# Kernel optimization log

Measured on AMD Instinct MI355X. Metric: run time of the kernel, lower is better.

The kernel has to match this reference:

```python
import jax, jax.numpy as jnp
import numpy as np

B, N, NDIM = 256, 127, 3          # batch, particles, input features
D, H, L, HID = 256, 8, 4, 256     # d_model, heads, layers, dim_feedforward(=nb_features=head hidden)
M = HID                           # Performer nb_features
DH = D // H                       # head dim
LN_EPS = 1e-5
KERN_EPS = 1e-4


def leaky(x):
    return jnp.where(x >= 0, x, 0.2 * x)


def layer_norm(x, g, b):
    mu = jnp.mean(x, axis=-1, keepdims=True)
    var = jnp.mean((x - mu) ** 2, axis=-1, keepdims=True)
    return (x - mu) * jax.lax.rsqrt(var + LN_EPS) * g + b


def softmax_kernel(data, proj, is_query):
    # FAVOR+ positive softmax random features (performer_pytorch.softmax_kernel)
    # data [B,H,S,DH], proj [M,DH]
    normalizer = DH ** -0.25
    ratio = proj.shape[0] ** -0.5
    dd = jnp.einsum('bhnd,md->bhnm', data * normalizer, proj)
    diag = jnp.sum(data ** 2, axis=-1, keepdims=True) * 0.5 * (normalizer ** 2)
    if is_query:
        mx = jax.lax.stop_gradient(jnp.max(dd, axis=-1, keepdims=True))
    else:
        mx = jax.lax.stop_gradient(jnp.max(dd))
    return ratio * (jnp.exp(dd - diag - mx) + KERN_EPS)


def performer_attn(h, keep, Wq, bq, Wk, bk, Wv, bv, Wo, bo, proj):
    Bc, S, _ = h.shape
    def split(y):
        return y.reshape(Bc, S, H, DH).transpose(0, 2, 1, 3)  # [B,H,S,DH]
    q = split(jnp.einsum('bnd,ed->bne', h, Wq) + bq)
    k = split(jnp.einsum('bnd,ed->bne', h, Wk) + bk)
    v = split(jnp.einsum('bnd,ed->bne', h, Wv) + bv) * keep   # zero padded values
    qp = softmax_kernel(q, proj, True)    # [B,H,S,M]
    kp = softmax_kernel(k, proj, False)   # [B,H,S,M]
    ksum = jnp.sum(kp, axis=2)                                   # [B,H,M]
    d_inv = 1.0 / jnp.einsum('bhnm,bhm->bhn', qp, ksum)          # [B,H,S]
    ctx = jnp.einsum('bhnm,bhnd->bhmd', kp, v)                   # [B,H,M,DH]
    o = jnp.einsum('bhmd,bhnm,bhn->bhnd', ctx, qp, d_inv)
    o = o.transpose(0, 2, 1, 3).reshape(Bc, S, D)
    return jnp.einsum('bnd,ed->bne', o, Wo) + bo


def encoder_layer(h, keep, Wq, bq, Wk, bk, Wv, bv, Wo, bo, proj,
                  n1w, n1b, n2w, n2b, f1w, f1b, f2w, f2b):
    # NOTE: the repo's override drops the residual connections (post-norm, no skip)
    a = performer_attn(h, keep, Wq, bq, Wk, bk, Wv, bv, Wo, bo, proj)
    h = layer_norm(a, n1w, n1b)
    f = jnp.einsum('bnh,dh->bnd', leaky(jnp.einsum('bnd,hd->bnh', h, f1w) + f1b), f2w) + f2b
    return layer_norm(f, n2w, n2b)


def setup_inputs():
    key = jax.random.key(0)
    ks = jax.random.split(key, 32)
    s = 0.02
    def w(k, shape):
        return jax.random.normal(k, shape, jnp.float32) * s
    return {
        'x': jax.random.normal(ks[0], (B, N, NDIM), jnp.float32),
        'mask': jax.random.randint(ks[1], (B, N), 0, 2) == 1,
        'emb_w': w(ks[2], (D, NDIM)), 'emb_b': w(ks[3], (D,)),
        'Wq': w(ks[4], (L, D, D)), 'bq': w(ks[5], (L, D)),
        'Wk': w(ks[6], (L, D, D)), 'bk': w(ks[7], (L, D)),
        'Wv': w(ks[8], (L, D, D)), 'bv': w(ks[9], (L, D)),
        'Wo': w(ks[10], (L, D, D)), 'bo': w(ks[11], (L, D)),
        'proj': jax.random.normal(ks[12], (L, M, DH), jnp.float32),
        'n1w': jnp.ones((L, D)), 'n1b': jnp.zeros((L, D)),
        'n2w': jnp.ones((L, D)), 'n2b': jnp.zeros((L, D)),
        'f1w': w(ks[13], (L, HID, D)), 'f1b': w(ks[14], (L, HID)),
        'f2w': w(ks[15], (L, D, HID)), 'f2b': w(ks[16], (L, D)),
        'h1w': w(ks[17], (2 * HID, D)), 'h1b': w(ks[18], (2 * HID,)),
        'h2w': w(ks[19], (HID, 2 * HID)), 'h2b': w(ks[20], (HID,)),
        'ow': w(ks[21], (1, HID)), 'ob': w(ks[22], (1,)),
    }


def reference(x, mask, emb_w, emb_b, Wq, bq, Wk, bk, Wv, bv, Wo, bo, proj,
              n1w, n1b, n2w, n2b, f1w, f1b, f2w, f2b,
              h1w, h1b, h2w, h2b, ow, ob):
    h = jnp.einsum('bnf,df->bnd', x, emb_w) + emb_b               # embed [B,N,D]
    h = jnp.concatenate([jnp.zeros_like(h[:, :1]), h], axis=1)    # prepend zero CLS token
    pad = jnp.concatenate([jnp.zeros_like(mask[:, :1]), mask], axis=1)  # [B,N+1], True=pad
    keep = (~pad).astype(h.dtype)[:, None, :, None]               # [B,1,S,1]
    for l in range(L):
        h = encoder_layer(h, keep, Wq[l], bq[l], Wk[l], bk[l], Wv[l], bv[l],
                          Wo[l], bo[l], proj[l], n1w[l], n1b[l], n2w[l], n2b[l],
                          f1w[l], f1b[l], f2w[l], f2b[l])
    c = h[:, 0]                                                   # CLS token [B,D]
    c = leaky(jnp.einsum('bd,hd->bh', c, h1w) + h1b)
    c = leaky(jnp.einsum('bh,gh->bg', c, h2w) + h2b)
    return jnp.einsum('bg,og->bo', c, ow) + ob                    # [B,1]
```

## Files before the change

kernel.cpp:

```cpp
#include <hip/hip_runtime.h>
#include <math.h>

#define B_ 256
#define N_ 127
#define S_ 128
#define NDIM_ 3
#define D_ 256
#define H_ 8
#define DH_ 32
#define M_ 256
#define HID_ 256
#define L_ 4
#define LOG2E 1.44269504088896340736f

typedef __attribute__((ext_vector_type(8))) short short8;
typedef __attribute__((ext_vector_type(4))) short bfx4;
typedef __attribute__((ext_vector_type(4))) float floatx4;

__device__ __forceinline__ ushort bf16_rn(float x) {
    unsigned u = __float_as_uint(x);
    u = (u + 0x7fffu + ((u >> 16) & 1u)) >> 16;
    return (ushort)u;
}
__device__ __forceinline__ unsigned split_pack(float x) {
    const ushort h = bf16_rn(x);
    const float r = x - __uint_as_float(((unsigned)h) << 16);
    const ushort l = bf16_rn(r);
    return (unsigned)h | ((unsigned)l << 16);
}
__device__ __forceinline__ float rec(unsigned u) {
    return __uint_as_float(u << 16) + __uint_as_float(u & 0xffff0000u);
}
__device__ __forceinline__ unsigned hpair(unsigned u0, unsigned u1) {
    return (u0 & 0xffffu) | (u1 << 16);
}
__device__ __forceinline__ unsigned lpair(unsigned u0, unsigned u1) {
    return (u0 >> 16) | (u1 & 0xffff0000u);
}

__device__ __forceinline__ float blk_sum(float v, float* sred) {
#pragma unroll
    for (int o = 32; o > 0; o >>= 1) v += __shfl_xor(v, o, 64);
    if ((threadIdx.x & 63) == 0) sred[threadIdx.x >> 6] = v;
    __syncthreads();
    v = sred[0] + sred[1] + sred[2] + sred[3];
    __syncthreads();
    return v;
}

__global__ void __launch_bounds__(256) k_prep(
    const float* __restrict__ Wq, const float* __restrict__ Wk, const float* __restrict__ Wv,
    const float* __restrict__ Wo, const float* __restrict__ f1w, const float* __restrict__ f2w,
    const float* __restrict__ proj, ushort* __restrict__ WH, ushort* __restrict__ WL,
    unsigned* __restrict__ P2, int* __restrict__ slots,
    const float* __restrict__ x, const float* __restrict__ ew, const float* __restrict__ eb,
    unsigned* __restrict__ Aout)
{
    const int bid = blockIdx.x;
    if (bid < 768) {
        const int tensor = bid / 128;
        const int tid = (bid & 127) * 256 + threadIdx.x;
        const float* src = tensor == 0 ? Wq : tensor == 1 ? Wk : tensor == 2 ? Wv
                         : tensor == 3 ? Wo : tensor == 4 ? f1w : f2w;
        ushort* dh = WH + (size_t)tensor * L_ * 65536;
        ushort* dl = WL + (size_t)tensor * L_ * 65536;
        const int l = tid >> 13;
        const int col = (tid >> 5) & 255, kc = tid & 31;
        const float* sp = src + ((size_t)l << 16) + col * 256 + kc * 8;
        float v[8];
        *(float4*)&v[0] = *(const float4*)sp;
        *(float4*)&v[4] = *(const float4*)(sp + 4);
        unsigned hu[4], lu[4];
#pragma unroll
        for (int i = 0; i < 4; i++) {
            const unsigned u0 = split_pack(v[2 * i]);
            const unsigned u1 = split_pack(v[2 * i + 1]);
            hu[i] = hpair(u0, u1);
            lu[i] = lpair(u0, u1);
        }
        const size_t off = ((size_t)l << 16) + ((size_t)(kc * 256 + col)) * 8;
        *(uint4*)&dh[off] = make_uint4(hu[0], hu[1], hu[2], hu[3]);
        *(uint4*)&dl[off] = make_uint4(lu[0], lu[1], lu[2], lu[3]);
    } else if (bid < 800) {
        const int idx = ((bid - 768) * 256 + threadIdx.x) * 4;
        const float4 w4 = *(const float4*)&proj[idx];
        const float v[4] = {w4.x, w4.y, w4.z, w4.w};
        unsigned u[4];
#pragma unroll
        for (int i = 0; i < 4; i++) u[i] = split_pack(v[i]);
        *(uint4*)&P2[idx] = make_uint4(u[0], u[1], u[2], u[3]);
    } else if (bid == 800) {
        if (threadIdx.x < 4) {
            const int i = __float_as_int(-INFINITY);
            slots[threadIdx.x] = (i >= 0) ? i : (i ^ 0x7fffffff);
        }
    } else {
        const int idx4 = (bid - 801) * 256 + threadIdx.x;
        const int d0 = (idx4 & 63) * 4;
        const int n = (idx4 >> 6) & (S_ - 1);
        const int b = idx4 >> 13;
        unsigned r[4] = {0u, 0u, 0u, 0u};
        if (n > 0) {
            const float* xr = x + ((size_t)b * N_ + (n - 1)) * NDIM_;
            const float x0 = xr[0], x1 = xr[1], x2 = xr[2];
#pragma unroll
            for (int j = 0; j < 4; j++) {
                const int d = d0 + j;
                const float val = eb[d] + x0 * ew[d * 3 + 0] + x1 * ew[d * 3 + 1] + x2 * ew[d * 3 + 2];
                r[j] = split_pack(val);
            }
        }
        *(uint4*)&Aout[(size_t)idx4 * 4] = make_uint4(r[0], r[1], r[2], r[3]);
    }
}

__global__ void __launch_bounds__(512, 2) k_gemm_qkv(
    const unsigned* __restrict__ Ap, const ushort* __restrict__ WHb,
    const ushort* __restrict__ WLb, const int l,
    const float* __restrict__ bq, const float* __restrict__ bk, const float* __restrict__ bv_,
    const int* __restrict__ mask,
    unsigned* __restrict__ Qo, unsigned* __restrict__ Ko, unsigned* __restrict__ Vo)
{
    __shared__ ushort sAh[2][4160];
    __shared__ ushort sAl[2][4160];
    const int t = threadIdx.x;
    const int w = t >> 6, lane = t & 63;
    const int quad = lane >> 4, l16 = lane & 15;
    const int rowbase = 64 * (w >> 2), colbase = 64 * (w & 3);
    const int which = blockIdx.x >> 8;
    const int row0 = (blockIdx.x & 255) * 128;
    const ushort* WH = WHb + ((size_t)(which * L_ + l)) * 65536;
    const ushort* WL = WLb + ((size_t)(which * L_ + l)) * 65536;
    const float* bias = which == 0 ? bq : which == 1 ? bk : bv_;
    unsigned* out = which == 0 ? Qo : which == 1 ? Ko : Vo;

    floatx4 acc[4][4];
#pragma unroll
    for (int rt = 0; rt < 4; rt++)
#pragma unroll
        for (int ct = 0; ct < 4; ct++) acc[rt][ct] = (floatx4){0.f, 0.f, 0.f, 0.f};

    const int arow = t >> 2, achunk = t & 3;
    const unsigned* AG = Ap + (size_t)(row0 + arow) * D_ + achunk * 8;
    const int aidx = achunk * 1040 + arow * 8;

    {
        const uint4 a0 = *(const uint4*)AG;
        const uint4 a1 = *(const uint4*)(AG + 4);
        *(uint4*)&sAh[0][aidx] = make_uint4(hpair(a0.x, a0.y), hpair(a0.z, a0.w),
                                            hpair(a1.x, a1.y), hpair(a1.z, a1.w));
        *(uint4*)&sAl[0][aidx] = make_uint4(lpair(a0.x, a0.y), lpair(a0.z, a0.w),
                                            lpair(a1.x, a1.y), lpair(a1.z, a1.w));
    }
    __syncthreads();

    for (int s = 0; s < 8; s++) {
        const int p = s & 1;
        uint4 a0n, a1n;
        if (s + 1 < 8) {
            a0n = *(const uint4*)(AG + (s + 1) * 32);
            a1n = *(const uint4*)(AG + (s + 1) * 32 + 4);
        }
        const size_t wbase = ((size_t)((s * 4 + quad) * 256 + colbase + l16)) * 8;
        const ushort* WHf = WH + wbase;
        const ushort* WLf = WL + wbase;
        short8 ah[4], al[4], wh[4], wl[4];
#pragma unroll
        for (int ct = 0; ct < 4; ct++) {
            wh[ct] = *(const short8*)&WHf[ct * 128];
            wl[ct] = *(const short8*)&WLf[ct * 128];
        }
#pragma unroll
        for (int rt = 0; rt < 4; rt++) {
            const int ai = quad * 1040 + (rowbase + 16 * rt + l16) * 8;
            ah[rt] = *(const short8*)&sAh[p][ai];
            al[rt] = *(const short8*)&sAl[p][ai];
        }
#pragma unroll
        for (int rt = 0; rt < 4; rt++)
#pragma unroll
            for (int ct = 0; ct < 4; ct++) {
                acc[rt][ct] = __builtin_amdgcn_mfma_f32_16x16x32_bf16(ah[rt], wh[ct], acc[rt][ct], 0, 0, 0);
                acc[rt][ct] = __builtin_amdgcn_mfma_f32_16x16x32_bf16(ah[rt], wl[ct], acc[rt][ct], 0, 0, 0);
                acc[rt][ct] = __builtin_amdgcn_mfma_f32_16x16x32_bf16(al[rt], wh[ct], acc[rt][ct], 0, 0, 0);
            }
        if (s + 1 < 8) {
            *(uint4*)&sAh[p ^ 1][aidx] = make_uint4(hpair(a0n.x, a0n.y), hpair(a0n.z, a0n.w),
                                                    hpair(a1n.x, a1n.y), hpair(a1n.z, a1n.w));
            *(uint4*)&sAl[p ^ 1][aidx] = make_uint4(lpair(a0n.x, a0n.y), lpair(a0n.z, a0n.w),
                                                    lpair(a1n.x, a1n.y), lpair(a1n.z, a1n.w));
        }
        __syncthreads();
    }

    int colv[4]; float bv[4];
#pragma unroll
    for (int ct = 0; ct < 4; ct++) { colv[ct] = colbase + 16 * ct + l16; bv[ct] = bias[colv[ct]]; }

    const int b = row0 >> 7;
#pragma unroll
    for (int rt = 0; rt < 4; rt++)
#pragma unroll
    for (int i = 0; i < 4; i++) {
        const int rl = rowbase + 16 * rt + quad * 4 + i;
        const int n = (row0 + rl) & (S_ - 1);
        float keep = 1.f;
        if (which == 2) keep = (n == 0) ? 1.f : (mask[b * N_ + n - 1] ? 0.f : 1.f);
#pragma unroll
        for (int ct = 0; ct < 4; ct++) {
            float c = acc[rt][ct][i] + bv[ct];
            c *= keep;
            const int col = colv[ct];
            out[(((size_t)b * H_ + (col >> 5)) * S_ + n) * DH_ + (col & 31)] = split_pack(c);
        }
    }
}

__global__ void __launch_bounds__(512, 2) k_wofn(
    const unsigned* __restrict__ Ap,
    const ushort* __restrict__ WoH, const ushort* __restrict__ WoL,
    const ushort* __restrict__ W1H, const ushort* __restrict__ W1L,
    const ushort* __restrict__ W2H, const ushort* __restrict__ W2L,
    const float* __restrict__ bo, const float* __restrict__ n1w, const float* __restrict__ n1b,
    const float* __restrict__ b1, const float* __restrict__ b2,
    const float* __restrict__ g2w, const float* __restrict__ g2b,
    unsigned* __restrict__ out)
{
    __shared__ char smemc[67584];
    ushort* Th  = (ushort*)smemc;
    ushort* Tl  = (ushort*)(smemc + 33792);
    ushort* sTh = (ushort*)smemc;
    ushort* sTl = (ushort*)(smemc + 8320);
    __shared__ float sredA[64][8], sredB[64][8];
    const int t = threadIdx.x;
    const int w = t >> 6, lane = t & 63;
    const int quad = lane >> 4, l16 = lane & 15;
    const int row0 = blockIdx.x * 64;

    floatx4 acc[2][4];
#pragma unroll
    for (int rt = 0; rt < 2; rt++)
#pragma unroll
        for (int ct = 0; ct < 4; ct++) acc[rt][ct] = (floatx4){0.f, 0.f, 0.f, 0.f};

    const int arow = t >> 3, akq = t & 7;
    const unsigned* AG = Ap + (size_t)(row0 + arow) * D_ + akq * 4;
    const int aidx = (akq >> 1) * 520 + arow * 8 + (akq & 1) * 4;

    {
        const uint4 a4 = *(const uint4*)AG;
        *(uint2*)&sTh[aidx] = make_uint2(hpair(a4.x, a4.y), hpair(a4.z, a4.w));
        *(uint2*)&sTl[aidx] = make_uint2(lpair(a4.x, a4.y), lpair(a4.z, a4.w));
    }
    __syncthreads();

    for (int s = 0; s < 8; s++) {
        const int p = s & 1;
        uint4 a_n;
        if (s + 1 < 8) a_n = *(const uint4*)(AG + (s + 1) * 32);
        const size_t wbase = ((size_t)((s * 4 + quad) * 256 + 32 * w + l16)) * 8;
        short8 fh[2], fl[2], th[4], tl[4];
#pragma unroll
        for (int rt = 0; rt < 2; rt++) {
            fh[rt] = *(const short8*)&WoH[wbase + rt * 128];
            fl[rt] = *(const short8*)&WoL[wbase + rt * 128];
        }
#pragma unroll
        for (int ct = 0; ct < 4; ct++) {
            const int ti = p * 2080 + quad * 520 + (16 * ct + l16) * 8;
            th[ct] = *(const short8*)&sTh[ti];
            tl[ct] = *(const short8*)&sTl[ti];
        }
#pragma unroll
        for (int rt = 0; rt < 2; rt++)
#pragma unroll
            for (int ct = 0; ct < 4; ct++) {
                acc[rt][ct] = __builtin_amdgcn_mfma_f32_16x16x32_bf16(fh[rt], th[ct], acc[rt][ct], 0, 0, 0);
                acc[rt][ct] = __builtin_amdgcn_mfma_f32_16x16x32_bf16(fl[rt], th[ct], acc[rt][ct], 0, 0, 0);
                acc[rt][ct] = __builtin_amdgcn_mfma_f32_16x16x32_bf16(fh[rt], tl[ct], acc[rt][ct], 0, 0, 0);
            }
        if (s + 1 < 8) {
            *(uint2*)&sTh[(p ^ 1) * 2080 + aidx] = make_uint2(hpair(a_n.x, a_n.y), hpair(a_n.z, a_n.w));
            *(uint2*)&sTl[(p ^ 1) * 2080 + aidx] = make_uint2(lpair(a_n.x, a_n.y), lpair(a_n.z, a_n.w));
        }
        __syncthreads();
    }

    {
        float bov[2][4];
#pragma unroll
        for (int rt = 0; rt < 2; rt++)
#pragma unroll
            for (int i = 0; i < 4; i++) bov[rt][i] = bo[32 * w + 16 * rt + quad * 4 + i];
        float ps[4], ps2[4];
#pragma unroll
        for (int ct = 0; ct < 4; ct++) { ps[ct] = 0.f; ps2[ct] = 0.f; }
#pragma unroll
        for (int rt = 0; rt < 2; rt++)
#pragma unroll
        for (int ct = 0; ct < 4; ct++)
#pragma unroll
        for (int i = 0; i < 4; i++) {
            const float c = acc[rt][ct][i] + bov[rt][i];
            acc[rt][ct][i] = c;
            ps[ct] += c; ps2[ct] += c * c;
        }
#pragma unroll
        for (int ct = 0; ct < 4; ct++) {
            ps[ct] += __shfl_xor(ps[ct], 16, 64);  ps[ct] += __shfl_xor(ps[ct], 32, 64);
            ps2[ct] += __shfl_xor(ps2[ct], 16, 64); ps2[ct] += __shfl_xor(ps2[ct], 32, 64);
        }
        if (quad == 0) {
#pragma unroll
            for (int ct = 0; ct < 4; ct++) {
                sredA[16 * ct + l16][w] = ps[ct];
                sredB[16 * ct + l16][w] = ps2[ct];
            }
        }
        __syncthreads();
        float mu[4], rs[4];
#pragma unroll
        for (int ct = 0; ct < 4; ct++) {
            const int n = 16 * ct + l16;
            float s = 0.f, s2 = 0.f;
#pragma unroll
            for (int k = 0; k < 8; k++) { s += sredA[n][k]; s2 += sredB[n][k]; }
            mu[ct] = s * (1.f / D_);
            rs[ct] = rsqrtf(s2 * (1.f / D_) - mu[ct] * mu[ct] + 1e-5f);
        }
        float gv1[2][4], bv1[2][4];
#pragma unroll
        for (int rt = 0; rt < 2; rt++)
#pragma unroll
            for (int i = 0; i < 4; i++) {
                const int c2 = 32 * w + 16 * rt + quad * 4 + i;
                gv1[rt][i] = n1w[c2];
                bv1[rt][i] = n1b[c2];
            }
#pragma unroll
        for (int ct = 0; ct < 4; ct++) {
            const int n = 16 * ct + l16;
#pragma unroll
            for (int rt = 0; rt < 2; rt++) {
                unsigned u[4];
#pragma unroll
                for (int i = 0; i < 4; i++) {
                    const float tv = (acc[rt][ct][i] - mu[ct]) * rs[ct] * gv1[rt][i] + bv1[rt][i];
                    u[i] = split_pack(tv);
                }
                const int base = n * 264 + 32 * w + 16 * rt + quad * 4;
                *(uint2*)&Th[base] = make_uint2(hpair(u[0], u[1]), hpair(u[2], u[3]));
                *(uint2*)&Tl[base] = make_uint2(lpair(u[0], u[1]), lpair(u[2], u[3]));
            }
        }
        __syncthreads();
    }

    floatx4 acc1[2][4];
#pragma unroll
    for (int rt = 0; rt < 2; rt++)
#pragma unroll
        for (int ct = 0; ct < 4; ct++) acc1[rt][ct] = (floatx4){0.f, 0.f, 0.f, 0.f};

    for (int s = 0; s < 8; s++) {
        const size_t wbase = ((size_t)((s * 4 + quad) * 256 + 32 * w + l16)) * 8;
        short8 fh[2], fl[2], th[4], tl[4];
#pragma unroll
        for (int rt = 0; rt < 2; rt++) {
            fh[rt] = *(const short8*)&W1H[wbase + rt * 128];
            fl[rt] = *(const short8*)&W1L[wbase + rt * 128];
        }
#pragma unroll
        for (int ct = 0; ct < 4; ct++) {
            const int ti = (16 * ct + l16) * 264 + s * 32 + quad * 8;
            th[ct] = *(const short8*)&Th[ti];
            tl[ct] = *(const short8*)&Tl[ti];
        }
#pragma unroll
        for (int rt = 0; rt < 2; rt++)
#pragma unroll
            for (int ct = 0; ct < 4; ct++) {
                acc1[rt][ct] = __builtin_amdgcn_mfma_f32_16x16x32_bf16(fh[rt], th[ct], acc1[rt][ct], 0, 0, 0);
                acc1[rt][ct] = __builtin_amdgcn_mfma_f32_16x16x32_bf16(fl[rt], th[ct], acc1[rt][ct], 0, 0, 0);
                acc1[rt][ct] = __builtin_amdgcn_mfma_f32_16x16x32_bf16(fh[rt], tl[ct], acc1[rt][ct], 0, 0, 0);
            }
    }
    __syncthreads();

    {
        float b1v[2][4];
#pragma unroll
        for (int rt = 0; rt < 2; rt++)
#pragma unroll
            for (int i = 0; i < 4; i++) b1v[rt][i] = b1[32 * w + 16 * rt + quad * 4 + i];
#pragma unroll
        for (int ct = 0; ct < 4; ct++) {
            const int n = 16 * ct + l16;
#pragma unroll
            for (int rt = 0; rt < 2; rt++) {
                unsigned u[4];
#pragma unroll
                for (int i = 0; i < 4; i++) {
                    float c = acc1[rt][ct][i] + b1v[rt][i];
                    c = (c >= 0.f) ? c : 0.2f * c;
                    u[i] = split_pack(c);
                }
                const int base = n * 264 + 32 * w + 16 * rt + quad * 4;
                *(uint2*)&Th[base] = make_uint2(hpair(u[0], u[1]), hpair(u[2], u[3]));
                *(uint2*)&Tl[base] = make_uint2(lpair(u[0], u[1]), lpair(u[2], u[3]));
            }
        }
        __syncthreads();
    }

    const int rowbase = 32 * (w >> 2), colbase = 64 * (w & 3);
    const int colg = w & 3;
    floatx4 acc2[2][4];
#pragma unroll
    for (int rt = 0; rt < 2; rt++)
#pragma unroll
        for (int ct = 0; ct < 4; ct++) acc2[rt][ct] = (floatx4){0.f, 0.f, 0.f, 0.f};

    for (int ks = 0; ks < 8; ks++) {
        const size_t w2base = ((size_t)((ks * 4 + quad) * 256 + colbase + l16)) * 8;
        short8 ah[2], al[2], wh[4], wl[4];
#pragma unroll
        for (int ct = 0; ct < 4; ct++) {
            wh[ct] = *(const short8*)&W2H[w2base + ct * 128];
            wl[ct] = *(const short8*)&W2L[w2base + ct * 128];
        }
#pragma unroll
        for (int rt = 0; rt < 2; rt++) {
            const int gi = (rowbase + 16 * rt + l16) * 264 + ks * 32 + quad * 8;
            ah[rt] = *(const short8*)&Th[gi];
            al[rt] = *(const short8*)&Tl[gi];
        }
#pragma unroll
        for (int rt = 0; rt < 2; rt++)
#pragma unroll
            for (int ct = 0; ct < 4; ct++) {
                acc2[rt][ct] = __builtin_amdgcn_mfma_f32_16x16x32_bf16(ah[rt], wh[ct], acc2[rt][ct], 0, 0, 0);
                acc2[rt][ct] = __builtin_amdgcn_mfma_f32_16x16x32_bf16(ah[rt], wl[ct], acc2[rt][ct], 0, 0, 0);
                acc2[rt][ct] = __builtin_amdgcn_mfma_f32_16x16x32_bf16(al[rt], wh[ct], acc2[rt][ct], 0, 0, 0);
            }
    }
    __syncthreads();

    int colv[4]; float bv[4], gv[4], bbv[4];
#pragma unroll
    for (int ct = 0; ct < 4; ct++) {
        colv[ct] = colbase + 16 * ct + l16;
        bv[ct] = b2[colv[ct]];
        gv[ct] = g2w[colv[ct]];
        bbv[ct] = g2b[colv[ct]];
    }
#pragma unroll
    for (int rt = 0; rt < 2; rt++)
#pragma unroll
    for (int i = 0; i < 4; i++) {
        const int rl = rowbase + 16 * rt + quad * 4 + i;
        float s = 0.f, s2 = 0.f;
#pragma unroll
        for (int ct = 0; ct < 4; ct++) {
            const float c = acc2[rt][ct][i] + bv[ct];
            s += c; s2 += c * c;
        }
#pragma unroll
        for (int o = 8; o > 0; o >>= 1) { s += __shfl_xor(s, o, 64); s2 += __shfl_xor(s2, o, 64); }
        if (l16 == 0) { sredA[rl][colg] = s; sredB[rl][colg] = s2; }
    }
    __syncthreads();
#pragma unroll
    for (int rt = 0; rt < 2; rt++)
#pragma unroll
    for (int i = 0; i < 4; i++) {
        const int rl = rowbase + 16 * rt + quad * 4 + i;
        const float s = sredA[rl][0] + sredA[rl][1] + sredA[rl][2] + sredA[rl][3];
        const float s2 = sredB[rl][0] + sredB[rl][1] + sredB[rl][2] + sredB[rl][3];
        const float mu = s * (1.f / D_);
        const float rs = rsqrtf(s2 * (1.f / D_) - mu * mu + 1e-5f);
#pragma unroll
        for (int ct = 0; ct < 4; ct++) {
            const float c = acc2[rt][ct][i] + bv[ct];
            out[(size_t)(row0 + rl) * D_ + colv[ct]] = split_pack((c - mu) * rs * gv[ct] + bbv[ct]);
        }
    }
}

__global__ void __launch_bounds__(256) k_dmax(
    const unsigned* __restrict__ kg, const unsigned* __restrict__ P2, int* __restrict__ slot)
{
    __shared__ __align__(16) ushort A2s[64 * 40];
    __shared__ __align__(16) ushort Ps[256 * 40];
    __shared__ float sred[4];
    const int t = threadIdx.x;
    const size_t row0 = (size_t)blockIdx.x * 64;
    {
        const int row = t >> 2, seg = t & 3;
        const unsigned* src = kg + (row0 + row) * DH_ + seg * 8;
        const uint4 f0 = *(const uint4*)src;
        const uint4 f1 = *(const uint4*)(src + 4);
        *(uint4*)&A2s[row * 40 + seg * 8] =
            make_uint4(hpair(f0.x, f0.y), hpair(f0.z, f0.w), hpair(f1.x, f1.y), hpair(f1.z, f1.w));
    }
    {
        const int col = t;
        const unsigned* src = P2 + (size_t)col * DH_;
#pragma unroll
        for (int hf = 0; hf < 2; hf++) {
            const uint4 g0 = *(const uint4*)(src + hf * 16);
            const uint4 g1 = *(const uint4*)(src + hf * 16 + 4);
            const uint4 g2 = *(const uint4*)(src + hf * 16 + 8);
            const uint4 g3 = *(const uint4*)(src + hf * 16 + 12);
            *(uint4*)&Ps[col * 40 + hf * 16] =
                make_uint4(hpair(g0.x, g0.y), hpair(g0.z, g0.w), hpair(g1.x, g1.y), hpair(g1.z, g1.w));
            *(uint4*)&Ps[col * 40 + hf * 16 + 8] =
                make_uint4(hpair(g2.x, g2.y), hpair(g2.z, g2.w), hpair(g3.x, g3.y), hpair(g3.z, g3.w));
        }
    }
    __syncthreads();
    const int w = t >> 6, lane = t & 63, quad = lane >> 4, l16 = lane & 15;
    floatx4 acc[4][4];
#pragma unroll
    for (int rt = 0; rt < 4; rt++)
#pragma unroll
        for (int ct = 0; ct < 4; ct++) acc[rt][ct] = (floatx4){0.f, 0.f, 0.f, 0.f};
    short8 af[4], bf[4];
#pragma unroll
    for (int rt = 0; rt < 4; rt++)
        af[rt] = *(const short8*)&A2s[(rt * 16 + l16) * 40 + quad * 8];
#pragma unroll
    for (int ct = 0; ct < 4; ct++)
        bf[ct] = *(const short8*)&Ps[((w * 4 + ct) * 16 + l16) * 40 + quad * 8];
#pragma unroll
    for (int rt = 0; rt < 4; rt++)
#pragma unroll
        for (int ct = 0; ct < 4; ct++)
            acc[rt][ct] = __builtin_amdgcn_mfma_f32_16x16x32_bf16(af[rt], bf[ct], acc[rt][ct], 0, 0, 0);
    float mx = -INFINITY;
#pragma unroll
    for (int rt = 0; rt < 4; rt++)
#pragma unroll
        for (int ct = 0; ct < 4; ct++)
#pragma unroll
            for (int i = 0; i < 4; i++) mx = fmaxf(mx, acc[rt][ct][i]);
#pragma unroll
    for (int o = 32; o > 0; o >>= 1) mx = fmaxf(mx, __shfl_xor(mx, o, 64));
    if (lane == 0) sred[w] = mx;
    __syncthreads();
    if (t == 0) {
        const float m4 = fmaxf(fmaxf(sred[0], sred[1]), fmaxf(sred[2], sred[3]))
                       * 0.42044820762685725f;
        const int i = __float_as_int(m4);
        atomicMax(slot, (i >= 0) ? i : (i ^ 0x7fffffff));
    }
}

__global__ void __launch_bounds__(1024) k_attn2(
    const unsigned* __restrict__ qg, const unsigned* __restrict__ kg, const unsigned* __restrict__ vg,
    const unsigned* __restrict__ P2, const int* __restrict__ slot,
    unsigned* __restrict__ outp)
{
    extern __shared__ char smem[];
    ushort* sAh   = (ushort*)(smem);
    ushort* sAl   = (ushort*)(smem + 10240);
    ushort* sBh   = (ushort*)(smem + 20480);
    ushort* sBl   = (ushort*)(smem + 25600);
    ushort* kpS   = (ushort*)(smem + 30720);
    ushort* sV    = (ushort*)(smem + 48128);
    ushort* sCtx  = (ushort*)(smem + 56832);
    float* sdk    = (float*)(smem + 73728);
    float* sdq    = (float*)(smem + 74240);
    float* smaxP  = (float*)(smem + 74752);
    float* sdenP  = smaxP;
    float* sksum  = (float*)(smem + 75776);
    float* sksP   = (float*)(smem + 76800);

    const int bh = blockIdx.x;
    const int b = bh >> 3, hh = bh & 7;
    const int t = threadIdx.x;
    const int w = t >> 6, lane = t & 63, quad = lane >> 4, l16 = lane & 15;
    const int wg = w & 7, wh = w >> 3;
    const int nq = wg * 16 + l16;
    const unsigned* kb = kg + (size_t)bh * S_ * DH_;
    const unsigned* qb = qg + (size_t)bh * S_ * DH_;
    const unsigned* vb = vg + (size_t)bh * S_ * DH_;
    const float nrm = 0.42044820762685725f;
    const float diagc = 0.5f * nrm * nrm;
    const float ratio = 0.0625f;

    union U8 { uint4 u; short8 s; };
    union U4 { uint2 u; bfx4 s; };

    float kmaxv;
    { const int iv = *slot; kmaxv = __int_as_float((iv >= 0) ? iv : (iv ^ 0x7fffffff)); }

    short8 qfh, qfl;
    {
        const unsigned* qrow = qb + (size_t)nq * DH_ + quad * 8;
        const uint4 q0 = *(const uint4*)qrow;
        const uint4 q1 = *(const uint4*)(qrow + 4);
        U8 th; th.u = make_uint4(hpair(q0.x, q0.y), hpair(q0.z, q0.w), hpair(q1.x, q1.y), hpair(q1.z, q1.w));
        U8 tl; tl.u = make_uint4(lpair(q0.x, q0.y), lpair(q0.z, q0.w), lpair(q1.x, q1.y), lpair(q1.z, q1.w));
        qfh = th.s; qfl = tl.s;
    }

    if (t < 512) {
        const int row = t >> 2, seg = t & 3;
        const unsigned* src = kb + row * DH_ + seg * 8;
        const uint4 f0 = *(const uint4*)&src[0];
        const uint4 f1 = *(const uint4*)&src[4];
        *(uint4*)&sAh[row * 40 + seg * 8] =
            make_uint4(hpair(f0.x, f0.y), hpair(f0.z, f0.w), hpair(f1.x, f1.y), hpair(f1.z, f1.w));
        *(uint4*)&sAl[row * 40 + seg * 8] =
            make_uint4(lpair(f0.x, f0.y), lpair(f0.z, f0.w), lpair(f1.x, f1.y), lpair(f1.z, f1.w));
    } else {
        const int tt2 = t - 512;
        const int n = tt2 & 127, d0 = (tt2 >> 7) * 8;
        const unsigned* src = vb + n * DH_ + d0;
        const uint4 f0 = *(const uint4*)&src[0];
        const uint4 f1 = *(const uint4*)&src[4];
        const unsigned uu[8] = {f0.x, f0.y, f0.z, f0.w, f1.x, f1.y, f1.z, f1.w};
#pragma unroll
        for (int j = 0; j < 8; j++)
            sV[(d0 + j) * 136 + n] = (ushort)(uu[j] & 0xffffu);
    }
    if (t < 128) {
        float s = 0.f, s2 = 0.f;
#pragma unroll
        for (int d4 = 0; d4 < DH_ / 4; d4++) {
            const uint4 kk = *(const uint4*)&kb[t * DH_ + d4 * 4];
            const float k0 = rec(kk.x), k1 = rec(kk.y), k2 = rec(kk.z), k3 = rec(kk.w);
            s += k0 * k0 + k1 * k1 + k2 * k2 + k3 * k3;
            const uint4 qq = *(const uint4*)&qb[t * DH_ + d4 * 4];
            const float q0 = rec(qq.x), q1 = rec(qq.y), q2 = rec(qq.z), q3 = rec(qq.w);
            s2 += q0 * q0 + q1 * q1 + q2 * q2 + q3 * q3;
        }
        sdk[t] = s * diagc + kmaxv;
        sdq[t] = s2 * diagc;
    }
    __syncthreads();

    floatx4 adq[2][4];
#pragma unroll
    for (int j = 0; j < 2; j++)
#pragma unroll
        for (int mtl = 0; mtl < 4; mtl++) adq[j][mtl] = (floatx4){0.f, 0.f, 0.f, 0.f};

#pragma unroll
    for (int qd = 0; qd < 4; qd++) {
        {
            const int col = t >> 4, ch2 = t & 15;
            const unsigned* src = P2 + (size_t)(qd * 64 + col) * DH_ + ch2 * 2;
            const unsigned u0 = src[0], u1 = src[1];
            ((unsigned*)sBh)[col * 20 + ch2] = hpair(u0, u1);
            ((unsigned*)sBl)[col * 20 + ch2] = lpair(u0, u1);
        }
        __syncthreads();
        floatx4 acc[2];
        acc[0] = (floatx4){0.f, 0.f, 0.f, 0.f};
        acc[1] = (floatx4){0.f, 0.f, 0.f, 0.f};
        {
            const short8 afh = *(const short8*)&sAh[nq * 40 + quad * 8];
            const short8 afl = *(const short8*)&sAl[nq * 40 + quad * 8];
#pragma unroll
            for (int ctl = 0; ctl < 2; ctl++) {
                const int mrow = ((2 * wh + ctl) * 16 + l16) * 40 + quad * 8;
                const short8 bfh = *(const short8*)&sBh[mrow];
                const short8 bfl = *(const short8*)&sBl[mrow];
                acc[ctl] = __builtin_amdgcn_mfma_f32_16x16x32_bf16(afh, bfh, acc[ctl], 0, 0, 0);
                acc[ctl] = __builtin_amdgcn_mfma_f32_16x16x32_bf16(afh, bfl, acc[ctl], 0, 0, 0);
                acc[ctl] = __builtin_amdgcn_mfma_f32_16x16x32_bf16(afl, bfh, acc[ctl], 0, 0, 0);
            }
        }
        float kc[2];
#pragma unroll
        for (int ctl = 0; ctl < 2; ctl++) {
            float kcl = 0.f;
            ushort kh[4];
#pragma unroll
            for (int i = 0; i < 4; i++) {
                const int n = wg * 16 + quad * 4 + i;
                const float kp = ratio * (__expf(acc[ctl][i] * nrm - sdk[n]) + 1e-4f);
                kh[i] = bf16_rn(kp);
                kcl += __uint_as_float((unsigned)kh[i] << 16);
            }
            *(uint2*)&kpS[((2 * wh + ctl) * 16 + l16) * 136 + wg * 16 + quad * 4] =
                make_uint2((unsigned)kh[0] | ((unsigned)kh[1] << 16),
                           (unsigned)kh[2] | ((unsigned)kh[3] << 16));
            kc[ctl] = kcl;
        }
#pragma unroll
        for (int ctl = 0; ctl < 2; ctl++) {
            kc[ctl] += __shfl_xor(kc[ctl], 16, 64);
            kc[ctl] += __shfl_xor(kc[ctl], 32, 64);
        }
        if (quad == 0) {
            sksP[w * 32 + l16] = kc[0];
            sksP[w * 32 + 16 + l16] = kc[1];
        }
        __syncthreads();
        const int qown = (qd & 1) ^ 1;
        if (wh == qown) {
            const int aidx2 = qd >> 1;
#pragma unroll
            for (int mtl = 0; mtl < 4; mtl++) {
                const int prow = (mtl * 16 + l16) * 40 + quad * 8;
                const short8 aPh = *(const short8*)&sBh[prow];
                const short8 aPl = *(const short8*)&sBl[prow];
                adq[aidx2][mtl] = __builtin_amdgcn_mfma_f32_16x16x32_bf16(aPh, qfh, adq[aidx2][mtl], 0, 0, 0);
                adq[aidx2][mtl] = __builtin_amdgcn_mfma_f32_16x16x32_bf16(aPh, qfl, adq[aidx2][mtl], 0, 0, 0);
                adq[aidx2][mtl] = __builtin_amdgcn_mfma_f32_16x16x32_bf16(aPl, qfh, adq[aidx2][mtl], 0, 0, 0);
            }
        } else {
            const int mt = wg & 3, dt = wg >> 2;
            floatx4 cacc = (floatx4){0.f, 0.f, 0.f, 0.f};
#pragma unroll
            for (int ks = 0; ks < 4; ks++) {
                const short8 a = *(const short8*)&kpS[(mt * 16 + l16) * 136 + ks * 32 + quad * 8];
                const short8 bvv = *(const short8*)&sV[(dt * 16 + l16) * 136 + ks * 32 + quad * 8];
                cacc = __builtin_amdgcn_mfma_f32_16x16x32_bf16(a, bvv, cacc, 0, 0, 0);
            }
            ushort ch[4];
#pragma unroll
            for (int i = 0; i < 4; i++) ch[i] = bf16_rn(cacc[i]);
            *(uint2*)&sCtx[(dt * 16 + l16) * 264 + qd * 64 + mt * 16 + quad * 4] =
                make_uint2((unsigned)ch[0] | ((unsigned)ch[1] << 16),
                           (unsigned)ch[2] | ((unsigned)ch[3] << 16));
        }
        if (t < 64) {
            float s = 0.f;
#pragma unroll
            for (int wg2 = 0; wg2 < 8; wg2++)
                s += sksP[((t >> 5) * 8 + wg2) * 32 + (t & 31)];
            sksum[qd * 64 + t] = s;
        }
        __syncthreads();
    }

    {
        float mxn = -INFINITY;
#pragma unroll
        for (int j = 0; j < 2; j++)
#pragma unroll
            for (int mtl = 0; mtl < 4; mtl++)
#pragma unroll
                for (int i = 0; i < 4; i++) mxn = fmaxf(mxn, adq[j][mtl][i]);
        mxn = fmaxf(mxn, __shfl_xor(mxn, 16, 64));
        mxn = fmaxf(mxn, __shfl_xor(mxn, 32, 64));
        if (quad == 0) smaxP[wh * 128 + nq] = mxn;
    }
    __syncthreads();
    const float dmq = sdq[nq] + fmaxf(smaxP[nq], smaxP[128 + nq]) * nrm;

    floatx4 oT[2];
    oT[0] = (floatx4){0.f, 0.f, 0.f, 0.f};
    oT[1] = (floatx4){0.f, 0.f, 0.f, 0.f};
    float dp = 0.f;
#pragma unroll
    for (int j = 0; j < 2; j++) {
        const int qdo = 2 * j + (wh ^ 1);
#pragma unroll
        for (int mtl = 0; mtl < 4; mtl++) {
            ushort qh[4];
#pragma unroll
            for (int i = 0; i < 4; i++) {
                const float qp = ratio * (__expf(adq[j][mtl][i] * nrm - dmq) + 1e-4f);
                qh[i] = bf16_rn(qp);
                dp += __uint_as_float((unsigned)qh[i] << 16)
                    * sksum[qdo * 64 + mtl * 16 + quad * 4 + i];
            }
            U4 tb;
            tb.u = make_uint2((unsigned)qh[0] | ((unsigned)qh[1] << 16),
                              (unsigned)qh[2] | ((unsigned)qh[3] << 16));
#pragma unroll
            for (int dt = 0; dt < 2; dt++) {
                U4 ta;
                ta.u = *(const uint2*)&sCtx[(dt * 16 + l16) * 264 + qdo * 64 + mtl * 16 + quad * 4];
                oT[dt] = __builtin_amdgcn_mfma_f32_16x16x16bf16_1k(ta.s, tb.s, oT[dt], 0, 0, 0);
            }
        }
    }
    dp += __shfl_xor(dp, 16, 64);
    dp += __shfl_xor(dp, 32, 64);
    __syncthreads();
    if (quad == 0) sdenP[wh * 128 + nq] = dp;

    float* oRed = (float*)kpS;
    if (wh == 1) {
#pragma unroll
        for (int dt = 0; dt < 2; dt++)
            *(floatx4*)&oRed[((wg * 2 + dt) * 64 + lane) * 4] = oT[dt];
    }
    __syncthreads();
    if (wh == 0) {
        const float inv = 1.0f / (sdenP[nq] + sdenP[128 + nq]);
#pragma unroll
        for (int dt = 0; dt < 2; dt++) {
            const floatx4 o2 = *(const floatx4*)&oRed[((wg * 2 + dt) * 64 + lane) * 4];
            const unsigned r0 = split_pack((oT[dt][0] + o2[0]) * inv);
            const unsigned r1 = split_pack((oT[dt][1] + o2[1]) * inv);
            const unsigned r2 = split_pack((oT[dt][2] + o2[2]) * inv);
            const unsigned r3 = split_pack((oT[dt][3] + o2[3]) * inv);
            *(uint4*)&outp[((size_t)b * S_ + nq) * D_ + hh * DH_ + dt * 16 + quad * 4] =
                make_uint4(r0, r1, r2, r3);
        }
    }
}

__global__ void __launch_bounds__(256) k_head(
    const unsigned* __restrict__ hfin, const float* __restrict__ h1w, const float* __restrict__ h1b,
    const float* __restrict__ h2w, const float* __restrict__ h2b,
    const float* __restrict__ ow, const float* __restrict__ ob, float* __restrict__ outp)
{
    __shared__ float c0[D_];
    __shared__ float c1[2 * HID_];
    __shared__ float sred[4];
    const int t = threadIdx.x;
    const int b = blockIdx.x;
    c0[t] = rec(hfin[(size_t)b * S_ * D_ + t]);
    __syncthreads();
#pragma unroll
    for (int half = 0; half < 2; half++) {
        const int j = half * 256 + t;
        float a = h1b[j];
        const float* w = h1w + (size_t)j * D_;
        for (int d = 0; d < D_; d += 4) {
            const float4 w4 = *(const float4*)&w[d];
            const float4 x4 = *(const float4*)&c0[d];
            a += x4.x * w4.x + x4.y * w4.y + x4.z * w4.z + x4.w * w4.w;
        }
        c1[j] = (a >= 0.f) ? a : 0.2f * a;
    }
    __syncthreads();
    float a2 = h2b[t];
    const float* w2 = h2w + (size_t)t * (2 * HID_);
    for (int j = 0; j < 2 * HID_; j += 4) {
        const float4 w4 = *(const float4*)&w2[j];
        const float4 x4 = *(const float4*)&c1[j];
        a2 += x4.x * w4.x + x4.y * w4.y + x4.z * w4.z + x4.w * w4.w;
    }
    const float c2 = (a2 >= 0.f) ? a2 : 0.2f * a2;
    const float s = blk_sum(c2 * ow[t], sred);
    if (t == 0) outp[b] = s + ob[0];
}

extern "C" void kernel_launch(void* const* d_in, const int* in_sizes, int n_in,
                              void* d_out, int out_size, void* d_ws, size_t ws_size,
                              hipStream_t stream)
{
    const float* x     = (const float*)d_in[0];
    const int*   mask  = (const int*)d_in[1];
    const float* emb_w = (const float*)d_in[2];
    const float* emb_b = (const float*)d_in[3];
    const float* Wq    = (const float*)d_in[4];
    const float* bq    = (const float*)d_in[5];
    const float* Wk    = (const float*)d_in[6];
    const float* bk    = (const float*)d_in[7];
    const float* Wv    = (const float*)d_in[8];
    const float* bv    = (const float*)d_in[9];
    const float* Wo    = (const float*)d_in[10];
    const float* bo    = (const float*)d_in[11];
    const float* proj  = (const float*)d_in[12];
    const float* n1w   = (const float*)d_in[13];
    const float* n1b   = (const float*)d_in[14];
    const float* n2w   = (const float*)d_in[15];
    const float* n2b   = (const float*)d_in[16];
    const float* f1w   = (const float*)d_in[17];
    const float* f1b   = (const float*)d_in[18];
    const float* f2w   = (const float*)d_in[19];
    const float* f2b   = (const float*)d_in[20];
    const float* h1w   = (const float*)d_in[21];
    const float* h1b   = (const float*)d_in[22];
    const float* h2w   = (const float*)d_in[23];
    const float* h2b   = (const float*)d_in[24];
    const float* ow    = (const float*)d_in[25];
    const float* ob    = (const float*)d_in[26];

    const size_t BSD = (size_t)B_ * S_ * D_;
    unsigned* A = (unsigned*)d_ws;
    unsigned* Q = A + BSD;
    unsigned* K = Q + BSD;
    unsigned* V = K + BSD;
    const size_t WMU = 65536;
    ushort* WH = (ushort*)(V + BSD);
    ushort* WL = WH + 6 * L_ * WMU;
    unsigned* P2 = (unsigned*)(WL + 6 * L_ * WMU);
    int* slots = (int*)(P2 + (size_t)L_ * M_ * DH_);

    k_prep<<<801 + 8192, 256, 0, stream>>>(Wq, Wk, Wv, Wo, f1w, f2w, proj, WH, WL, P2, slots,
                                           x, emb_w, emb_b, A);

    const int GB2 = B_ * S_ / 128;
    const int DB = B_ * H_ * S_ / 64;
    const size_t ATTN_LDS = 78848;

    for (int l = 0; l < L_; l++) {
        const unsigned* P2l = P2 + (size_t)l * M_ * DH_;
        k_gemm_qkv<<<3 * GB2, 512, 0, stream>>>(A, WH, WL, l, bq + l * D_, bk + l * D_, bv + l * D_, mask, Q, K, V);
        k_dmax<<<DB, 256, 0, stream>>>(K, P2l, slots + l);
        k_attn2<<<B_ * H_, 1024, ATTN_LDS, stream>>>(Q, K, V, P2l, slots + l, A);
        k_wofn<<<B_ * S_ / 64, 512, 0, stream>>>(A,
            WH + (3 * L_ + l) * WMU, WL + (3 * L_ + l) * WMU,
            WH + (4 * L_ + l) * WMU, WL + (4 * L_ + l) * WMU,
            WH + (5 * L_ + l) * WMU, WL + (5 * L_ + l) * WMU,
            bo + l * D_, n1w + l * D_, n1b + l * D_,
            f1b + l * HID_, f2b + l * D_, n2w + l * D_, n2b + l * D_, A);
    }
    k_head<<<B_, 256, 0, stream>>>(A, h1w, h1b, h2w, h2b, ow, ob, (float*)d_out);
}
```

Baseline: 1.155 ms.

## Load activation tile once per block and loop over Q, K, V weights

The QKV GEMM previously launched one block per (projection, 128-row tile), so each A tile was read from global memory and split into hi/lo bf16 three times. Now each block loads a 64-row A tile in full into LDS once and computes Q, K and V in turn, with 512 blocks instead of 768. This removes repeated A reads and conversions but drops the double-buffered K-loop prefetch. It also halves the rows per wave, which lowers MFMA reuse of the weight fragments, and fewer blocks may reduce occupancy.

New measurement: 1.173 ms. No clear change (+1.6%).

```diff
diff --git a/kernel.cpp b/kernel.cpp
--- a/kernel.cpp
+++ b/kernel.cpp
@@ -121,97 +121,90 @@
     const int* __restrict__ mask,
     unsigned* __restrict__ Qo, unsigned* __restrict__ Ko, unsigned* __restrict__ Vo)
 {
-    __shared__ ushort sAh[2][4160];
-    __shared__ ushort sAl[2][4160];
+    __shared__ ushort sAh[32 * 520];
+    __shared__ ushort sAl[32 * 520];
     const int t = threadIdx.x;
     const int w = t >> 6, lane = t & 63;
     const int quad = lane >> 4, l16 = lane & 15;
-    const int rowbase = 64 * (w >> 2), colbase = 64 * (w & 3);
-    const int which = blockIdx.x >> 8;
-    const int row0 = (blockIdx.x & 255) * 128;
-    const ushort* WH = WHb + ((size_t)(which * L_ + l)) * 65536;
-    const ushort* WL = WLb + ((size_t)(which * L_ + l)) * 65536;
-    const float* bias = which == 0 ? bq : which == 1 ? bk : bv_;
-    unsigned* out = which == 0 ? Qo : which == 1 ? Ko : Vo;
-
-    floatx4 acc[4][4];
-#pragma unroll
-    for (int rt = 0; rt < 4; rt++)
-#pragma unroll
-        for (int ct = 0; ct < 4; ct++) acc[rt][ct] = (floatx4){0.f, 0.f, 0.f, 0.f};
-
-    const int arow = t >> 2, achunk = t & 3;
-    const unsigned* AG = Ap + (size_t)(row0 + arow) * D_ + achunk * 8;
-    const int aidx = achunk * 1040 + arow * 8;
+    const int rowbase = 32 * (w >> 2), colbase = 64 * (w & 3);
+    const int row0 = blockIdx.x * 64;
 
     {
-        const uint4 a0 = *(const uint4*)AG;
-        const uint4 a1 = *(const uint4*)(AG + 4);
-        *(uint4*)&sAh[0][aidx] = make_uint4(hpair(a0.x, a0.y), hpair(a0.z, a0.w),
-                                            hpair(a1.x, a1.y), hpair(a1.z, a1.w));
-        *(uint4*)&sAl[0][aidx] = make_uint4(lpair(a0.x, a0.y), lpair(a0.z, a0.w),
-                                            lpair(a1.x, a1.y), lpair(a1.z, a1.w));
-    }
-    __syncthreads();
-
-    for (int s = 0; s < 8; s++) {
-        const int p = s & 1;
-        uint4 a0n, a1n;
-        if (s + 1 < 8) {
-            a0n = *(const uint4*)(AG + (s + 1) * 32);
-            a1n = *(const uint4*)(AG + (s + 1) * 32 + 4);
-        }
-        const size_t wbase = ((size_t)((s * 4 + quad) * 256 + colbase + l16)) * 8;
-        const ushort* WHf = WH + wbase;
-        const ushort* WLf = WL + wbase;
-        short8 ah[4], al[4], wh[4], wl[4];
-#pragma unroll
-        for (int ct = 0; ct < 4; ct++) {
-            wh[ct] = *(const short8*)&WHf[ct * 128];
-            wl[ct] = *(const short8*)&WLf[ct * 128];
-        }
-#pragma unroll
-        for (int rt = 0; rt < 4; rt++) {
-            const int ai = quad * 1040 + (rowbase + 16 * rt + l16) * 8;
-            ah[rt] = *(const short8*)&sAh[p][ai];
-            al[rt] = *(const short8*)&sAl[p][ai];
-        }
-#pragma unroll
-        for (int rt = 0; rt < 4; rt++)
+        const int row = t >> 3, kcg = (t & 7) * 4;
+        const unsigned* arow = Ap + (size_t)(row0 + row) * D_;
+#pragma unroll
+        for (int j = 0; j < 4; j++) {
+            const int kc = kcg + j;
+            const unsigned* src = arow + kc * 8;
+            const uint4 a0 = *(const uint4*)src;
+            const uint4 a1 = *(const uint4*)(src + 4);
+            const int ai = kc * 520 + row * 8;
+            *(uint4*)&sAh[ai] = make_uint4(hpair(a0.x, a0.y), hpair(a0.z, a0.w),
+                                           hpair(a1.x, a1.y), hpair(a1.z, a1.w));
+            *(uint4*)&sAl[ai] = make_uint4(lpair(a0.x, a0.y), lpair(a0.z, a0.w),
+                                           lpair(a1.x, a1.y), lpair(a1.z, a1.w));
+        }
+    }
+    __syncthreads();
+
+    const int b = row0 >> 7;
+#pragma unroll
+    for (int which = 0; which < 3; which++) {
+        const ushort* WH = WHb + ((size_t)(which * L_ + l)) * 65536;
+        const ushort* WL = WLb + ((size_t)(which * L_ + l)) * 65536;
+        const float* bias = which == 0 ? bq : which == 1 ? bk : bv_;
+        unsigned* out = which == 0 ? Qo : which == 1 ? Ko : Vo;
+
+        floatx4 acc[2][4];
+#pragma unroll
+        for (int rt = 0; rt < 2; rt++)
+#pragma unroll
+            for (int ct = 0; ct < 4; ct++) acc[rt][ct] = (floatx4){0.f, 0.f, 0.f, 0.f};
+
+        for (int s = 0; s < 8; s++) {
+            const size_t wbase = ((size_t)((s * 4 + quad) * 256 + colbase + l16)) * 8;
+            const ushort* WHf = WH + wbase;
+            const ushort* WLf = WL + wbase;
+            short8 ah[2], al[2], wh[4], wl[4];
 #pragma unroll
             for (int ct = 0; ct < 4; ct++) {
-                acc[rt][ct] = __builtin_amdgcn_mfma_f32_16x16x32_bf16(ah[rt], wh[ct], acc[rt][ct], 0, 0, 0);
-                acc[rt][ct] = __builtin_amdgcn_mfma_f32_16x16x32_bf16(ah[rt], wl[ct], acc[rt][ct], 0, 0, 0);
-                acc[rt][ct] = __builtin_amdgcn_mfma_f32_16x16x32_bf16(al[rt], wh[ct], acc[rt][ct], 0, 0, 0);
-            }
-        if (s + 1 < 8) {
-            *(uint4*)&sAh[p ^ 1][aidx] = make_uint4(hpair(a0n.x, a0n.y), hpair(a0n.z, a0n.w),
-                                                    hpair(a1n.x, a1n.y), hpair(a1n.z, a1n.w));
-            *(uint4*)&sAl[p ^ 1][aidx] = make_uint4(lpair(a0n.x, a0n.y), lpair(a0n.z, a0n.w),
-                                                    lpair(a1n.x, a1n.y), lpair(a1n.z, a1n.w));
-        }
-        __syncthreads();
-    }
-
-    int colv[4]; float bv[4];
-#pragma unroll
-    for (int ct = 0; ct < 4; ct++) { colv[ct] = colbase + 16 * ct + l16; bv[ct] = bias[colv[ct]]; }
-
-    const int b = row0 >> 7;
-#pragma unroll
-    for (int rt = 0; rt < 4; rt++)
-#pragma unroll
-    for (int i = 0; i < 4; i++) {
-        const int rl = rowbase + 16 * rt + quad * 4 + i;
-        const int n = (row0 + rl) & (S_ - 1);
-        float keep = 1.f;
-        if (which == 2) keep = (n == 0) ? 1.f : (mask[b * N_ + n - 1] ? 0.f : 1.f);
-#pragma unroll
-        for (int ct = 0; ct < 4; ct++) {
-            float c = acc[rt][ct][i] + bv[ct];
-            c *= keep;
-            const int col = colv[ct];
-            out[(((size_t)b * H_ + (col >> 5)) * S_ + n) * DH_ + (col & 31)] = split_pack(c);
+                wh[ct] = *(const short8*)&WHf[ct * 128];
+                wl[ct] = *(const short8*)&WLf[ct * 128];
+            }
+#pragma unroll
+            for (int rt = 0; rt < 2; rt++) {
+                const int ai = (s * 4 + quad) * 520 + (rowbase + 16 * rt + l16) * 8;
+                ah[rt] = *(const short8*)&sAh[ai];
+                al[rt] = *(const short8*)&sAl[ai];
+            }
+#pragma unroll
+            for (int rt = 0; rt < 2; rt++)
+#pragma unroll
+                for (int ct = 0; ct < 4; ct++) {
+                    acc[rt][ct] = __builtin_amdgcn_mfma_f32_16x16x32_bf16(ah[rt], wh[ct], acc[rt][ct], 0, 0, 0);
+                    acc[rt][ct] = __builtin_amdgcn_mfma_f32_16x16x32_bf16(ah[rt], wl[ct], acc[rt][ct], 0, 0, 0);
+                    acc[rt][ct] = __builtin_amdgcn_mfma_f32_16x16x32_bf16(al[rt], wh[ct], acc[rt][ct], 0, 0, 0);
+                }
+        }
+
+        int colv[4]; float bv[4];
+#pragma unroll
+        for (int ct = 0; ct < 4; ct++) { colv[ct] = colbase + 16 * ct + l16; bv[ct] = bias[colv[ct]]; }
+#pragma unroll
+        for (int rt = 0; rt < 2; rt++)
+#pragma unroll
+        for (int i = 0; i < 4; i++) {
+            const int rl = rowbase + 16 * rt + quad * 4 + i;
+            const int n = (row0 + rl) & (S_ - 1);
+            float keep = 1.f;
+            if (which == 2) keep = (n == 0) ? 1.f : (mask[b * N_ + n - 1] ? 0.f : 1.f);
+#pragma unroll
+            for (int ct = 0; ct < 4; ct++) {
+                float c = acc[rt][ct][i] + bv[ct];
+                if (which == 2) c *= keep;
+                const int col = colv[ct];
+                out[(((size_t)b * H_ + (col >> 5)) * S_ + n) * DH_ + (col & 31)] = split_pack(c);
+            }
         }
     }
 }
@@ -891,13 +884,13 @@
     k_prep<<<801 + 8192, 256, 0, stream>>>(Wq, Wk, Wv, Wo, f1w, f2w, proj, WH, WL, P2, slots,
                                            x, emb_w, emb_b, A);
 
-    const int GB2 = B_ * S_ / 128;
+    const int QB = B_ * S_ / 64;
     const int DB = B_ * H_ * S_ / 64;
     const size_t ATTN_LDS = 78848;
 
     for (int l = 0; l < L_; l++) {
         const unsigned* P2l = P2 + (size_t)l * M_ * DH_;
-        k_gemm_qkv<<<3 * GB2, 512, 0, stream>>>(A, WH, WL, l, bq + l * D_, bk + l * D_, bv + l * D_, mask, Q, K, V);
+        k_gemm_qkv<<<QB, 512, 0, stream>>>(A, WH, WL, l, bq + l * D_, bk + l * D_, bv + l * D_, mask, Q, K, V);
         k_dmax<<<DB, 256, 0, stream>>>(K, P2l, slots + l);
         k_attn2<<<B_ * H_, 1024, ATTN_LDS, stream>>>(Q, K, V, P2l, slots + l, A);
         k_wofn<<<B_ * S_ / 64, 512, 0, stream>>>(A,
```
